# Optimization experiments

Hardware: AMD Instinct MI355X
Metric: run time of the kernel (lower is better)

Reference implementation:

```python
import jax, jax.numpy as jnp
import numpy as np

B, S, E, H = 8, 2048, 1024, 64

def setup_inputs() -> dict:
    key = jax.random.key(0)
    ks = jax.random.split(key, 7)
    scale = 1.0 / np.sqrt(E)
    return {
        "x": jax.random.normal(ks[0], (B, S, E), dtype=jnp.float32),
        "mask": jnp.ones((B, S), dtype=jnp.int32),
        "Wq": jax.random.uniform(ks[1], (E, H), jnp.float32, -scale, scale),
        "bq": jax.random.uniform(ks[2], (H,), jnp.float32, -scale, scale),
        "Wk": jax.random.uniform(ks[3], (E, H), jnp.float32, -scale, scale),
        "bk": jax.random.uniform(ks[4], (H,), jnp.float32, -scale, scale),
        "Wv": jax.random.uniform(ks[5], (E, H), jnp.float32, -scale, scale),
        "bv": jax.random.uniform(ks[6], (H,), jnp.float32, -scale, scale),
    }

def reference(x, mask, Wq, bq, Wk, bk, Wv, bv):
    # q,k,v: [B,S,H]
    q = jnp.einsum('bse,eh->bsh', x, Wq) + bq
    k = jnp.einsum('bse,eh->bsh', x, Wk) + bk
    v = jnp.einsum('bse,eh->bsh', x, Wv) + bv
    # scores: [B,S,S]
    scores = jnp.einsum('bqh,bkh->bqk', q, k) / jnp.sqrt(jnp.asarray(H, q.dtype))
    causal = jnp.tril(jnp.ones((S, S), dtype=bool))  # [S,S]
    pad = (mask != 0)[:, None, :]                    # [B,1,S]
    neg_inf = jnp.asarray(float('-inf'), scores.dtype)
    scores = jnp.where(causal[None] & pad, scores, neg_inf)
    attn = jax.nn.softmax(scores, axis=-1)
    return jnp.einsum('bqk,bkh->bqh', attn, v)
```

## Files before the change

kernel.cpp:

```cpp
#include <hip/hip_runtime.h>
#include <hip/hip_bf16.h>

#define S_ 2048
#define E_ 1024
#define QNC 16

typedef __attribute__((ext_vector_type(8))) short short8;
typedef __attribute__((ext_vector_type(4))) float f32x4;

__device__ __forceinline__ short f2bf(float f) {
    __hip_bfloat16 h = __float2bfloat16(f);
    return *(short*)&h;
}

__device__ __forceinline__ void g2l16(const void* g, void* l) {
    __builtin_amdgcn_global_load_lds(
        (const __attribute__((address_space(1))) void*)g,
        (__attribute__((address_space(3))) void*)l, 16, 0, 0);
}

__global__ __launch_bounds__(256) void prep_weights(
    const float* __restrict__ Wq, const float* __restrict__ Wk,
    const float* __restrict__ Wv, unsigned short* __restrict__ Wt)
{
    int idx = blockIdx.x * 256 + threadIdx.x;
    int n = idx >> 10, k = idx & (E_ - 1);
    const float* W = (n < 64) ? Wq : (n < 128) ? Wk : Wv;
    Wt[idx] = (unsigned short)f2bf(W[k * 64 + (n & 63)]);
}

__global__ __launch_bounds__(256, 2) void qkv_main(
    const float* __restrict__ x, const unsigned short* __restrict__ Wt,
    const float* __restrict__ bq, const float* __restrict__ bk,
    const float* __restrict__ bv,
    unsigned short* __restrict__ Q, unsigned short* __restrict__ K,
    unsigned short* __restrict__ Vt)
{
    __shared__ __align__(16) char pool[2][32768];
    int tid = threadIdx.x;
    int wave = tid >> 6, lane = tid & 63;
    int lo = lane & 15, hi = lane >> 4;
    int wm = wave >> 1, wn = wave & 1;
    int rowbase = blockIdx.x * 32;
    const char* xg = (const char*)x;
    const char* wg = (const char*)Wt;

    f32x4 acc[6];
    #pragma unroll
    for (int j = 0; j < 6; ++j) acc[j] = (f32x4){0.f, 0.f, 0.f, 0.f};

    #define STAGE(bb, kc)                                                         \
        {                                                                         \
            _Pragma("unroll")                                                     \
            for (int i = 0; i < 2; ++i) {                                         \
                int u_lin = i * 256 + tid;                                        \
                int r = u_lin >> 4, u = u_lin & 15;                               \
                const char* src = xg + (size_t)(rowbase + r) * 4096 + (kc) * 256  \
                                  + (((u & 8) | ((u & 7) ^ (r & 7))) << 4);       \
                g2l16(src, &pool[bb][(i * 256 + wave * 64) * 16]);                \
            }                                                                     \
            _Pragma("unroll")                                                     \
            for (int i = 0; i < 6; ++i) {                                         \
                int u_lin = i * 256 + tid;                                        \
                int c = u_lin >> 3, u = u_lin & 7;                                \
                const char* src = wg + (size_t)c * 2048 + (kc) * 128              \
                                  + ((u ^ (c & 7)) << 4);                         \
                g2l16(src, &pool[bb][8192 + (i * 256 + wave * 64) * 16]);         \
            }                                                                     \
        }

    STAGE(0, 0);
    asm volatile("s_waitcnt vmcnt(0)" ::: "memory");
    __builtin_amdgcn_sched_barrier(0);
    __builtin_amdgcn_s_barrier();

    for (int t = 0; t < QNC; ++t) {
        if (t + 1 < QNC) STAGE((t + 1) & 1, t + 1);

        const char* lx = pool[t & 1];
        const char* lw = pool[t & 1] + 8192;
        int r = wm * 16 + lo;
        #pragma unroll
        for (int kk = 0; kk < 2; ++kk) {
            int u0 = kk * 8 + hi * 2;
            float4 a0 = *(const float4*)(lx + r * 256
                + (((u0 & 8) | ((u0 & 7) ^ (r & 7))) << 4));
            float4 a1 = *(const float4*)(lx + r * 256
                + ((((u0 + 1) & 8) | (((u0 + 1) & 7) ^ (r & 7))) << 4));
            short8 af;
            af[0] = f2bf(a0.x); af[1] = f2bf(a0.y);
            af[2] = f2bf(a0.z); af[3] = f2bf(a0.w);
            af[4] = f2bf(a1.x); af[5] = f2bf(a1.y);
            af[6] = f2bf(a1.z); af[7] = f2bf(a1.w);
            #pragma unroll
            for (int j = 0; j < 6; ++j) {
                int c = wn * 96 + j * 16 + lo;
                short8 bf = *(const short8*)(lw + c * 128
                    + (((kk * 4 + hi) ^ (c & 7)) << 4));
                acc[j] = __builtin_amdgcn_mfma_f32_16x16x32_bf16(af, bf, acc[j], 0, 0, 0);
            }
        }

        __builtin_amdgcn_sched_barrier(0);
        asm volatile("s_waitcnt vmcnt(0)" ::: "memory");
        __builtin_amdgcn_sched_barrier(0);
        __builtin_amdgcn_s_barrier();
    }
    #undef STAGE

    char* eq = pool[0];
    unsigned short* ev = (unsigned short*)pool[1];
    #pragma unroll
    for (int j = 0; j < 6; ++j) {
        int n = wn * 96 + j * 16 + lo;
        #pragma unroll
        for (int rr4 = 0; rr4 < 4; ++rr4) {
            int rr = wm * 16 + 4 * hi + rr4;
            float v = acc[j][rr4];
            if (n < 64) {
                *(unsigned short*)(eq + rr * 272 + n * 2) =
                    (unsigned short)f2bf(v + bq[n]);
            } else if (n < 128) {
                *(unsigned short*)(eq + rr * 272 + n * 2) =
                    (unsigned short)f2bf(v + bk[n - 64]);
            } else {
                ev[(n - 128) * 40 + rr] = (unsigned short)f2bf(v + bv[n - 128]);
            }
        }
    }
    __syncthreads();

    {
        #pragma unroll
        for (int i = 0; i < 2; ++i) {
            int u_lin = i * 256 + tid;
            int row = u_lin >> 4, seg = u_lin & 15;
            short8 val = *(const short8*)(eq + row * 272 + seg * 16);
            if (seg < 8)
                *(short8*)(Q + (size_t)(rowbase + row) * 64 + seg * 8) = val;
            else
                *(short8*)(K + (size_t)(rowbase + row) * 64 + (seg - 8) * 8) = val;
        }
        int h = tid >> 2, su = tid & 3;
        int b = rowbase >> 11, sl0 = rowbase & (S_ - 1);
        short8 val = *(const short8*)(ev + h * 40 + su * 8);
        *(short8*)(Vt + ((size_t)(b * 64 + h)) * S_ + sl0 + su * 8) = val;
    }
}

__global__ __launch_bounds__(256) void attn_stage(
    const unsigned short* __restrict__ Q, const unsigned short* __restrict__ K,
    const unsigned short* __restrict__ Vt, const int* __restrict__ mask,
    float* __restrict__ part)
{
    __shared__ __align__(16) char kv[3][16384];
    __shared__ __align__(16) unsigned short p_lds[4][16][72];
    int tid = threadIdx.x;
    int wave = tid >> 6, lane = tid & 63;
    int lo = lane & 15, hi = lane >> 4;
    int blk = blockIdx.x;
    int c = blk & 3;
    int pr = blk >> 2;
    int b = pr & 7;
    int qt64 = 31 - (pr >> 3);
    int nkt = qt64 + 1;
    int chunk = (nkt + 3) >> 2;
    int kt0 = c * chunk;
    int kt1 = min(kt0 + chunk, nkt);
    int ntile = kt1 - kt0;
    int qrow0 = qt64 * 64 + wave * 16;

    f32x4 o[4];
    float ps[4] = {0.f, 0.f, 0.f, 0.f};
    #pragma unroll
    for (int i = 0; i < 4; ++i) o[i] = (f32x4){0.f, 0.f, 0.f, 0.f};

    #define ASTAGE(bb, kt)                                                        \
        {                                                                         \
            int kbase_ = (kt) * 64;                                               \
            const char* kg = (const char*)K + (size_t)(b * S_ + kbase_) * 128;    \
            const char* vg = (const char*)Vt + (size_t)b * 64 * 4096 + kbase_ * 2;\
            _Pragma("unroll")                                                     \
            for (int j = 0; j < 2; ++j) {                                         \
                int r = (j * 4 + wave) * 8 + (lane >> 3);                         \
                int un = lane & 7;                                                \
                g2l16(kg + r * 128 + ((un ^ (r & 7)) << 4),                       \
                      &kv[bb][(j * 4 + wave) * 1024]);                            \
                g2l16(vg + (size_t)r * 4096 + ((un ^ (r & 7)) << 4),              \
                      &kv[bb][8192 + (j * 4 + wave) * 1024]);                     \
            }                                                                     \
        }

    if (ntile > 0) {
        const unsigned short* qp = Q + ((size_t)(b * S_ + qrow0 + lo)) * 64 + 8 * hi;
        short8 qf0 = *(const short8*)(qp);
        short8 qf1 = *(const short8*)(qp + 32);

        unsigned mbits = 0;
        for (int tt = 0; tt < 8; ++tt) {
            if (tt < ntile) {
                int kbase = (kt0 + tt) * 64;
                #pragma unroll
                for (int nt = 0; nt < 4; ++nt)
                    if (mask[b * S_ + kbase + nt * 16 + lo] != 0)
                        mbits |= (1u << (tt * 4 + nt));
            }
        }
        asm volatile("s_waitcnt vmcnt(0)" ::: "memory");
        __builtin_amdgcn_sched_barrier(0);

        ASTAGE(0, kt0);
        if (ntile > 1) ASTAGE(1, kt0 + 1);
        __builtin_amdgcn_sched_barrier(0);
        if (ntile > 1) asm volatile("s_waitcnt vmcnt(4)" ::: "memory");
        else           asm volatile("s_waitcnt vmcnt(0)" ::: "memory");
        __builtin_amdgcn_sched_barrier(0);
        __builtin_amdgcn_s_barrier();

        for (int t = 0; t < ntile; ++t) {
            int kbase = (kt0 + t) * 64;
            const char* kb = kv[t % 3];
            const char* vb = kv[t % 3] + 8192;

            f32x4 s[4];
            #pragma unroll
            for (int i = 0; i < 4; ++i) s[i] = (f32x4){0.f, 0.f, 0.f, 0.f};
            #pragma unroll
            for (int nt = 0; nt < 4; ++nt) {
                short8 kf0 = *(const short8*)(kb + (nt * 16 + lo) * 128 + ((hi ^ (lo & 7)) << 4));
                short8 kf1 = *(const short8*)(kb + (nt * 16 + lo) * 128 + (((4 + hi) ^ (lo & 7)) << 4));
                s[nt] = __builtin_amdgcn_mfma_f32_16x16x32_bf16(qf0, kf0, s[nt], 0, 0, 0);
                s[nt] = __builtin_amdgcn_mfma_f32_16x16x32_bf16(qf1, kf1, s[nt], 0, 0, 0);
            }

            #pragma unroll
            for (int nt = 0; nt < 4; ++nt) {
                int kpos = kbase + nt * 16 + lo;
                bool mok = (mbits >> (t * 4 + nt)) & 1;
                #pragma unroll
                for (int r = 0; r < 4; ++r) {
                    int qpos = qrow0 + 4 * hi + r;
                    bool ok = mok && (kpos <= qpos);
                    float pv = ok ? __expf(s[nt][r] * 0.125f) : 0.f;
                    ps[r] += pv;
                    p_lds[wave][4 * hi + r][nt * 16 + lo] = (unsigned short)f2bf(pv);
                }
            }

            #pragma unroll
            for (int kk = 0; kk < 2; ++kk) {
                short8 pf = *(const short8*)&p_lds[wave][lo][kk * 32 + 8 * hi];
                #pragma unroll
                for (int nt = 0; nt < 4; ++nt) {
                    short8 vf = *(const short8*)(vb + (nt * 16 + lo) * 128
                                                 + (((kk * 4 + hi) ^ (lo & 7)) << 4));
                    o[nt] = __builtin_amdgcn_mfma_f32_16x16x32_bf16(pf, vf, o[nt], 0, 0, 0);
                }
            }

            if (t + 2 < ntile) ASTAGE((t + 2) % 3, kt0 + t + 2);
            __builtin_amdgcn_sched_barrier(0);
            if (t + 1 < ntile) {
                if (t + 2 < ntile) asm volatile("s_waitcnt vmcnt(4)" ::: "memory");
                else               asm volatile("s_waitcnt vmcnt(0)" ::: "memory");
                __builtin_amdgcn_sched_barrier(0);
                __builtin_amdgcn_s_barrier();
            }
        }
    }
    #undef ASTAGE

    float l[4];
    #pragma unroll
    for (int r = 0; r < 4; ++r) {
        float v = ps[r];
        v += __shfl_xor(v, 1);
        v += __shfl_xor(v, 2);
        v += __shfl_xor(v, 4);
        v += __shfl_xor(v, 8);
        l[r] = v;
    }

    int tile16 = b * 128 + qt64 * 4 + wave;
    float* pp = part + (((size_t)c * 1024 + tile16) * 64 + lane) * 20;
    #pragma unroll
    for (int nt = 0; nt < 4; ++nt) *(f32x4*)(pp + nt * 4) = o[nt];
    f32x4 ll;
    #pragma unroll
    for (int r = 0; r < 4; ++r) ll[r] = l[r];
    *(f32x4*)(pp + 16) = ll;
}

__global__ __launch_bounds__(256) void attn_comb(
    const float* __restrict__ part, float* __restrict__ out)
{
    int g = blockIdx.x * 256 + threadIdx.x;
    int tile = g >> 6, lane = g & 63;
    int lo = lane & 15, hi = lane >> 4;
    int b = tile >> 7, qt = tile & 127;
    int qrow0 = qt * 16;

    f32x4 o[4];
    float l[4] = {0.f, 0.f, 0.f, 0.f};
    #pragma unroll
    for (int i = 0; i < 4; ++i) o[i] = (f32x4){0.f, 0.f, 0.f, 0.f};

    #pragma unroll
    for (int c = 0; c < 4; ++c) {
        const float* pp = part + (((size_t)c * 1024 + tile) * 64 + lane) * 20;
        #pragma unroll
        for (int nt = 0; nt < 4; ++nt) {
            f32x4 po = *(const f32x4*)(pp + nt * 4);
            #pragma unroll
            for (int r = 0; r < 4; ++r) o[nt][r] += po[r];
        }
        f32x4 pl = *(const f32x4*)(pp + 16);
        #pragma unroll
        for (int r = 0; r < 4; ++r) l[r] += pl[r];
    }

    #pragma unroll
    for (int nt = 0; nt < 4; ++nt) {
        #pragma unroll
        for (int r = 0; r < 4; ++r) {
            int qpos = qrow0 + 4 * hi + r;
            out[((size_t)(b * S_ + qpos)) * 64 + nt * 16 + lo] =
                (l[r] > 0.f) ? o[nt][r] / l[r] : 0.f;
        }
    }
}

extern "C" void kernel_launch(void* const* d_in, const int* in_sizes, int n_in,
                              void* d_out, int out_size, void* d_ws, size_t ws_size,
                              hipStream_t stream) {
    const float* x   = (const float*)d_in[0];
    const int*   msk = (const int*)d_in[1];
    const float* Wq  = (const float*)d_in[2];
    const float* bq  = (const float*)d_in[3];
    const float* Wk  = (const float*)d_in[4];
    const float* bk  = (const float*)d_in[5];
    const float* Wv  = (const float*)d_in[6];
    const float* bv  = (const float*)d_in[7];
    float* outp = (float*)d_out;

    char* w = (char*)d_ws;
    unsigned short* Wt = (unsigned short*)w;
    unsigned short* Qb = (unsigned short*)(w + 0x080000);
    unsigned short* Kb = (unsigned short*)(w + 0x280000);
    unsigned short* Vt = (unsigned short*)(w + 0x480000);
    float* partp = (float*)(w + 0x680000);

    prep_weights<<<dim3(768), dim3(256), 0, stream>>>(Wq, Wk, Wv, Wt);
    qkv_main<<<dim3(512), dim3(256), 0, stream>>>(x, Wt, bq, bk, bv, Qb, Kb, Vt);
    attn_stage<<<dim3(1024), dim3(256), 0, stream>>>(Qb, Kb, Vt, msk, partp);
    attn_comb<<<dim3(256), dim3(256), 0, stream>>>(partp, outp);
}
```

Before: 58.32 us.

## Split QKV projection columns across two blocks and triple-buffer K-loop staging

The QKV projection kernel now launches twice as many blocks, each computing 96 of the 192 output columns for a 32-row tile, which halves per-block accumulators and weight staging. The LDS pipeline moves from double to triple buffering with a two-stage prefetch and partial vmcnt waits, so loads for chunk t+2 overlap compute on chunk t. The aim is more parallelism and better latency hiding in the memory-bound projection. In exchange, each x tile is now loaded twice (once per column half), which adds global traffic for the dominant input, and the epilogue writes are split by half.

```diff
diff --git a/kernel.cpp b/kernel.cpp
--- a/kernel.cpp
+++ b/kernel.cpp
@@ -36,18 +36,20 @@
     unsigned short* __restrict__ Q, unsigned short* __restrict__ K,
     unsigned short* __restrict__ Vt)
 {
-    __shared__ __align__(16) char pool[2][32768];
+    __shared__ __align__(16) char pool[3][20480];
     int tid = threadIdx.x;
     int wave = tid >> 6, lane = tid & 63;
     int lo = lane & 15, hi = lane >> 4;
     int wm = wave >> 1, wn = wave & 1;
-    int rowbase = blockIdx.x * 32;
+    int rb = blockIdx.x >> 1, ch = blockIdx.x & 1;
+    int rowbase = rb * 32;
+    int colbase = ch * 96;
     const char* xg = (const char*)x;
     const char* wg = (const char*)Wt;
 
-    f32x4 acc[6];
-    #pragma unroll
-    for (int j = 0; j < 6; ++j) acc[j] = (f32x4){0.f, 0.f, 0.f, 0.f};
+    f32x4 acc[3];
+    #pragma unroll
+    for (int j = 0; j < 3; ++j) acc[j] = (f32x4){0.f, 0.f, 0.f, 0.f};
 
     #define STAGE(bb, kc)                                                         \
         {                                                                         \
@@ -60,25 +62,25 @@
                 g2l16(src, &pool[bb][(i * 256 + wave * 64) * 16]);                \
             }                                                                     \
             _Pragma("unroll")                                                     \
-            for (int i = 0; i < 6; ++i) {                                         \
+            for (int i = 0; i < 3; ++i) {                                         \
                 int u_lin = i * 256 + tid;                                        \
-                int c = u_lin >> 3, u = u_lin & 7;                                \
-                const char* src = wg + (size_t)c * 2048 + (kc) * 128              \
-                                  + ((u ^ (c & 7)) << 4);                         \
+                int cl = u_lin >> 3, u = u_lin & 7;                               \
+                const char* src = wg + (size_t)(colbase + cl) * 2048 + (kc) * 128 \
+                                  + ((u ^ (cl & 7)) << 4);                        \
                 g2l16(src, &pool[bb][8192 + (i * 256 + wave * 64) * 16]);         \
             }                                                                     \
         }
 
-    STAGE(0, 0);
-    asm volatile("s_waitcnt vmcnt(0)" ::: "memory");
+    STAGE(0, 0); STAGE(1, 1);
+    asm volatile("s_waitcnt vmcnt(5)" ::: "memory");
     __builtin_amdgcn_sched_barrier(0);
     __builtin_amdgcn_s_barrier();
 
     for (int t = 0; t < QNC; ++t) {
-        if (t + 1 < QNC) STAGE((t + 1) & 1, t + 1);
-
-        const char* lx = pool[t & 1];
-        const char* lw = pool[t & 1] + 8192;
+        if (t + 2 < QNC) STAGE((t + 2) % 3, t + 2);
+
+        const char* lx = pool[t % 3];
+        const char* lw = pool[t % 3] + 8192;
         int r = wm * 16 + lo;
         #pragma unroll
         for (int kk = 0; kk < 2; ++kk) {
@@ -93,35 +95,40 @@
             af[4] = f2bf(a1.x); af[5] = f2bf(a1.y);
             af[6] = f2bf(a1.z); af[7] = f2bf(a1.w);
             #pragma unroll
-            for (int j = 0; j < 6; ++j) {
-                int c = wn * 96 + j * 16 + lo;
-                short8 bf = *(const short8*)(lw + c * 128
-                    + (((kk * 4 + hi) ^ (c & 7)) << 4));
+            for (int j = 0; j < 3; ++j) {
+                int cl = wn * 48 + j * 16 + lo;
+                short8 bf = *(const short8*)(lw + cl * 128
+                    + (((kk * 4 + hi) ^ (cl & 7)) << 4));
                 acc[j] = __builtin_amdgcn_mfma_f32_16x16x32_bf16(af, bf, acc[j], 0, 0, 0);
             }
         }
 
         __builtin_amdgcn_sched_barrier(0);
-        asm volatile("s_waitcnt vmcnt(0)" ::: "memory");
-        __builtin_amdgcn_sched_barrier(0);
-        __builtin_amdgcn_s_barrier();
+        if (t + 2 < QNC)      asm volatile("s_waitcnt vmcnt(5)" ::: "memory");
+        else if (t + 1 < QNC) asm volatile("s_waitcnt vmcnt(0)" ::: "memory");
+        if (t + 1 < QNC) {
+            __builtin_amdgcn_sched_barrier(0);
+            __builtin_amdgcn_s_barrier();
+        }
     }
     #undef STAGE
 
+    __syncthreads();
     char* eq = pool[0];
     unsigned short* ev = (unsigned short*)pool[1];
     #pragma unroll
-    for (int j = 0; j < 6; ++j) {
-        int n = wn * 96 + j * 16 + lo;
-        #pragma unroll
-        for (int rr4 = 0; rr4 < 4; ++rr4) {
-            int rr = wm * 16 + 4 * hi + rr4;
-            float v = acc[j][rr4];
+    for (int j = 0; j < 3; ++j) {
+        int nl = wn * 48 + j * 16 + lo;
+        int n = colbase + nl;
+        #pragma unroll
+        for (int r4 = 0; r4 < 4; ++r4) {
+            int rr = wm * 16 + 4 * hi + r4;
+            float v = acc[j][r4];
             if (n < 64) {
-                *(unsigned short*)(eq + rr * 272 + n * 2) =
+                *(unsigned short*)(eq + rr * 208 + nl * 2) =
                     (unsigned short)f2bf(v + bq[n]);
             } else if (n < 128) {
-                *(unsigned short*)(eq + rr * 272 + n * 2) =
+                *(unsigned short*)(eq + rr * 208 + nl * 2) =
                     (unsigned short)f2bf(v + bk[n - 64]);
             } else {
                 ev[(n - 128) * 40 + rr] = (unsigned short)f2bf(v + bv[n - 128]);
@@ -130,21 +137,29 @@
     }
     __syncthreads();
 
-    {
-        #pragma unroll
-        for (int i = 0; i < 2; ++i) {
-            int u_lin = i * 256 + tid;
-            int row = u_lin >> 4, seg = u_lin & 15;
-            short8 val = *(const short8*)(eq + row * 272 + seg * 16);
-            if (seg < 8)
-                *(short8*)(Q + (size_t)(rowbase + row) * 64 + seg * 8) = val;
-            else
-                *(short8*)(K + (size_t)(rowbase + row) * 64 + (seg - 8) * 8) = val;
-        }
-        int h = tid >> 2, su = tid & 3;
-        int b = rowbase >> 11, sl0 = rowbase & (S_ - 1);
-        short8 val = *(const short8*)(ev + h * 40 + su * 8);
-        *(short8*)(Vt + ((size_t)(b * 64 + h)) * S_ + sl0 + su * 8) = val;
+    if (ch == 0) {
+        {
+            int row = tid >> 3, seg = tid & 7;
+            short8 val = *(const short8*)(eq + row * 208 + seg * 16);
+            *(short8*)(Q + (size_t)(rowbase + row) * 64 + seg * 8) = val;
+        }
+        if (tid < 128) {
+            int row = tid >> 2, seg = tid & 3;
+            short8 val = *(const short8*)(eq + row * 208 + 128 + seg * 16);
+            *(short8*)(K + (size_t)(rowbase + row) * 64 + seg * 8) = val;
+        }
+    } else {
+        if (tid < 128) {
+            int row = tid >> 2, seg = tid & 3;
+            short8 val = *(const short8*)(eq + row * 208 + seg * 16);
+            *(short8*)(K + (size_t)(rowbase + row) * 64 + 32 + seg * 8) = val;
+        }
+        {
+            int h = tid >> 2, su = tid & 3;
+            int b = rowbase >> 11, sl0 = rowbase & (S_ - 1);
+            short8 val = *(const short8*)(ev + h * 40 + su * 8);
+            *(short8*)(Vt + ((size_t)(b * 64 + h)) * S_ + sl0 + su * 8) = val;
+        }
     }
 }
 
@@ -351,7 +366,7 @@
     float* partp = (float*)(w + 0x680000);
 
     prep_weights<<<dim3(768), dim3(256), 0, stream>>>(Wq, Wk, Wv, Wt);
-    qkv_main<<<dim3(512), dim3(256), 0, stream>>>(x, Wt, bq, bk, bv, Qb, Kb, Vt);
+    qkv_main<<<dim3(1024), dim3(256), 0, stream>>>(x, Wt, bq, bk, bv, Qb, Kb, Vt);
     attn_stage<<<dim3(1024), dim3(256), 0, stream>>>(Qb, Kb, Vt, msk, partp);
     attn_comb<<<dim3(256), dim3(256), 0, stream>>>(partp, outp);
 }
```

Result: slower. 76.03 us (+30.4%).

## Double QKV projection row tile and use triple-buffered prefetch

Applied to the files above, without the earlier changes.

The QKV projection kernel now processes 64 rows per block instead of 32. Each wave computes two 16-row tiles that reuse the same loaded weight fragments, which halves weight LDS and global traffic per row. The LDS pipeline moves from double to triple buffering with two stages in flight, using partial vmcnt waits. In exchange the grid shrinks to 256 blocks at one block per CU, lowering occupancy and parallelism on a 256-CU part.

```diff
diff --git a/kernel.cpp b/kernel.cpp
--- a/kernel.cpp
+++ b/kernel.cpp
@@ -29,30 +29,32 @@
     Wt[idx] = (unsigned short)f2bf(W[k * 64 + (n & 63)]);
 }
 
-__global__ __launch_bounds__(256, 2) void qkv_main(
+__global__ __launch_bounds__(256, 1) void qkv_main(
     const float* __restrict__ x, const unsigned short* __restrict__ Wt,
     const float* __restrict__ bq, const float* __restrict__ bk,
     const float* __restrict__ bv,
     unsigned short* __restrict__ Q, unsigned short* __restrict__ K,
     unsigned short* __restrict__ Vt)
 {
-    __shared__ __align__(16) char pool[2][32768];
+    __shared__ __align__(16) char pool[3][40960];
     int tid = threadIdx.x;
     int wave = tid >> 6, lane = tid & 63;
     int lo = lane & 15, hi = lane >> 4;
     int wm = wave >> 1, wn = wave & 1;
-    int rowbase = blockIdx.x * 32;
+    int rowbase = blockIdx.x * 64;
     const char* xg = (const char*)x;
     const char* wg = (const char*)Wt;
 
-    f32x4 acc[6];
-    #pragma unroll
-    for (int j = 0; j < 6; ++j) acc[j] = (f32x4){0.f, 0.f, 0.f, 0.f};
+    f32x4 acc[2][6];
+    #pragma unroll
+    for (int a = 0; a < 2; ++a)
+        #pragma unroll
+        for (int j = 0; j < 6; ++j) acc[a][j] = (f32x4){0.f, 0.f, 0.f, 0.f};
 
     #define STAGE(bb, kc)                                                         \
         {                                                                         \
             _Pragma("unroll")                                                     \
-            for (int i = 0; i < 2; ++i) {                                         \
+            for (int i = 0; i < 4; ++i) {                                         \
                 int u_lin = i * 256 + tid;                                        \
                 int r = u_lin >> 4, u = u_lin & 15;                               \
                 const char* src = xg + (size_t)(rowbase + r) * 4096 + (kc) * 256  \
@@ -62,69 +64,83 @@
             _Pragma("unroll")                                                     \
             for (int i = 0; i < 6; ++i) {                                         \
                 int u_lin = i * 256 + tid;                                        \
-                int c = u_lin >> 3, u = u_lin & 7;                                \
-                const char* src = wg + (size_t)c * 2048 + (kc) * 128              \
-                                  + ((u ^ (c & 7)) << 4);                         \
-                g2l16(src, &pool[bb][8192 + (i * 256 + wave * 64) * 16]);         \
+                int cl = u_lin >> 3, u = u_lin & 7;                               \
+                const char* src = wg + (size_t)cl * 2048 + (kc) * 128             \
+                                  + ((u ^ (cl & 7)) << 4);                        \
+                g2l16(src, &pool[bb][16384 + (i * 256 + wave * 64) * 16]);        \
             }                                                                     \
         }
 
-    STAGE(0, 0);
-    asm volatile("s_waitcnt vmcnt(0)" ::: "memory");
+    STAGE(0, 0); STAGE(1, 1);
+    asm volatile("s_waitcnt vmcnt(10)" ::: "memory");
     __builtin_amdgcn_sched_barrier(0);
     __builtin_amdgcn_s_barrier();
 
     for (int t = 0; t < QNC; ++t) {
-        if (t + 1 < QNC) STAGE((t + 1) & 1, t + 1);
-
-        const char* lx = pool[t & 1];
-        const char* lw = pool[t & 1] + 8192;
-        int r = wm * 16 + lo;
+        if (t + 2 < QNC) STAGE((t + 2) % 3, t + 2);
+
+        const char* lx = pool[t % 3];
+        const char* lw = pool[t % 3] + 16384;
         #pragma unroll
         for (int kk = 0; kk < 2; ++kk) {
-            int u0 = kk * 8 + hi * 2;
-            float4 a0 = *(const float4*)(lx + r * 256
-                + (((u0 & 8) | ((u0 & 7) ^ (r & 7))) << 4));
-            float4 a1 = *(const float4*)(lx + r * 256
-                + ((((u0 + 1) & 8) | (((u0 + 1) & 7) ^ (r & 7))) << 4));
-            short8 af;
-            af[0] = f2bf(a0.x); af[1] = f2bf(a0.y);
-            af[2] = f2bf(a0.z); af[3] = f2bf(a0.w);
-            af[4] = f2bf(a1.x); af[5] = f2bf(a1.y);
-            af[6] = f2bf(a1.z); af[7] = f2bf(a1.w);
+            short8 bf[6];
             #pragma unroll
             for (int j = 0; j < 6; ++j) {
-                int c = wn * 96 + j * 16 + lo;
-                short8 bf = *(const short8*)(lw + c * 128
-                    + (((kk * 4 + hi) ^ (c & 7)) << 4));
-                acc[j] = __builtin_amdgcn_mfma_f32_16x16x32_bf16(af, bf, acc[j], 0, 0, 0);
+                int cl = wn * 96 + j * 16 + lo;
+                bf[j] = *(const short8*)(lw + cl * 128
+                    + (((kk * 4 + hi) ^ (cl & 7)) << 4));
+            }
+            #pragma unroll
+            for (int rt = 0; rt < 2; ++rt) {
+                int r = wm * 32 + rt * 16 + lo;
+                int u0 = kk * 8 + hi * 2;
+                float4 a0 = *(const float4*)(lx + r * 256
+                    + (((u0 & 8) | ((u0 & 7) ^ (r & 7))) << 4));
+                float4 a1 = *(const float4*)(lx + r * 256
+                    + ((((u0 + 1) & 8) | (((u0 + 1) & 7) ^ (r & 7))) << 4));
+                short8 af;
+                af[0] = f2bf(a0.x); af[1] = f2bf(a0.y);
+                af[2] = f2bf(a0.z); af[3] = f2bf(a0.w);
+                af[4] = f2bf(a1.x); af[5] = f2bf(a1.y);
+                af[6] = f2bf(a1.z); af[7] = f2bf(a1.w);
+                #pragma unroll
+                for (int j = 0; j < 6; ++j)
+                    acc[rt][j] = __builtin_amdgcn_mfma_f32_16x16x32_bf16(
+                        af, bf[j], acc[rt][j], 0, 0, 0);
             }
         }
 
         __builtin_amdgcn_sched_barrier(0);
-        asm volatile("s_waitcnt vmcnt(0)" ::: "memory");
-        __builtin_amdgcn_sched_barrier(0);
-        __builtin_amdgcn_s_barrier();
+        if (t + 2 < QNC)      asm volatile("s_waitcnt vmcnt(10)" ::: "memory");
+        else if (t + 1 < QNC) asm volatile("s_waitcnt vmcnt(0)" ::: "memory");
+        if (t + 1 < QNC) {
+            __builtin_amdgcn_sched_barrier(0);
+            __builtin_amdgcn_s_barrier();
+        }
     }
     #undef STAGE
 
+    __syncthreads();
     char* eq = pool[0];
-    unsigned short* ev = (unsigned short*)pool[1];
-    #pragma unroll
-    for (int j = 0; j < 6; ++j) {
-        int n = wn * 96 + j * 16 + lo;
-        #pragma unroll
-        for (int rr4 = 0; rr4 < 4; ++rr4) {
-            int rr = wm * 16 + 4 * hi + rr4;
-            float v = acc[j][rr4];
-            if (n < 64) {
-                *(unsigned short*)(eq + rr * 272 + n * 2) =
-                    (unsigned short)f2bf(v + bq[n]);
-            } else if (n < 128) {
-                *(unsigned short*)(eq + rr * 272 + n * 2) =
-                    (unsigned short)f2bf(v + bk[n - 64]);
-            } else {
-                ev[(n - 128) * 40 + rr] = (unsigned short)f2bf(v + bv[n - 128]);
+    unsigned short* ev = (unsigned short*)pool[2];
+    #pragma unroll
+    for (int rt = 0; rt < 2; ++rt) {
+        #pragma unroll
+        for (int j = 0; j < 6; ++j) {
+            int n = wn * 96 + j * 16 + lo;
+            #pragma unroll
+            for (int r4 = 0; r4 < 4; ++r4) {
+                int rr = wm * 32 + rt * 16 + 4 * hi + r4;
+                float v = acc[rt][j][r4];
+                if (n < 64) {
+                    *(unsigned short*)(eq + rr * 272 + n * 2) =
+                        (unsigned short)f2bf(v + bq[n]);
+                } else if (n < 128) {
+                    *(unsigned short*)(eq + rr * 272 + n * 2) =
+                        (unsigned short)f2bf(v + bk[n - 64]);
+                } else {
+                    ev[(n - 128) * 72 + rr] = (unsigned short)f2bf(v + bv[n - 128]);
+                }
             }
         }
     }
@@ -132,7 +148,7 @@
 
     {
         #pragma unroll
-        for (int i = 0; i < 2; ++i) {
+        for (int i = 0; i < 4; ++i) {
             int u_lin = i * 256 + tid;
             int row = u_lin >> 4, seg = u_lin & 15;
             short8 val = *(const short8*)(eq + row * 272 + seg * 16);
@@ -141,10 +157,14 @@
             else
                 *(short8*)(K + (size_t)(rowbase + row) * 64 + (seg - 8) * 8) = val;
         }
-        int h = tid >> 2, su = tid & 3;
         int b = rowbase >> 11, sl0 = rowbase & (S_ - 1);
-        short8 val = *(const short8*)(ev + h * 40 + su * 8);
-        *(short8*)(Vt + ((size_t)(b * 64 + h)) * S_ + sl0 + su * 8) = val;
+        #pragma unroll
+        for (int i = 0; i < 2; ++i) {
+            int u_lin = i * 256 + tid;
+            int h = u_lin >> 3, su = u_lin & 7;
+            short8 val = *(const short8*)(ev + h * 72 + su * 8);
+            *(short8*)(Vt + ((size_t)(b * 64 + h)) * S_ + sl0 + su * 8) = val;
+        }
     }
 }
 
@@ -351,7 +371,7 @@
     float* partp = (float*)(w + 0x680000);
 
     prep_weights<<<dim3(768), dim3(256), 0, stream>>>(Wq, Wk, Wv, Wt);
-    qkv_main<<<dim3(512), dim3(256), 0, stream>>>(x, Wt, bq, bk, bv, Qb, Kb, Vt);
+    qkv_main<<<dim3(256), dim3(256), 0, stream>>>(x, Wt, bq, bk, bv, Qb, Kb, Vt);
     attn_stage<<<dim3(1024), dim3(256), 0, stream>>>(Qb, Kb, Vt, msk, partp);
     attn_comb<<<dim3(256), dim3(256), 0, stream>>>(partp, outp);
 }
```

After: 65.83 us. 12.9% more time.

## Halve QKV projection row tile and K-chunk to raise occupancy

Applied to the files above, without the earlier changes.

The QKV projection kernel now processes 16 rows per block instead of 32 and stages 32-element K chunks, giving 32 pipeline steps instead of 16. Each of the four waves owns 48 output columns. LDS per block shrinks to about 28KB, which lets the launch bounds ask for 4 blocks per CU, and the grid doubles to 1024 blocks. The aim is more parallelism and better latency hiding. In exchange, every block reloads the full bf16 weight matrix, so total weight traffic through L2 doubles, and there are more barrier steps per row. The V-transpose LDS buffer now uses an 18-element row stride, so its 16-byte reads are not 16-byte aligned.

```diff
diff --git a/kernel.cpp b/kernel.cpp
--- a/kernel.cpp
+++ b/kernel.cpp
@@ -3,7 +3,7 @@
 
 #define S_ 2048
 #define E_ 1024
-#define QNC 16
+#define QNC 32
 
 typedef __attribute__((ext_vector_type(8))) short short8;
 typedef __attribute__((ext_vector_type(4))) float f32x4;
@@ -29,43 +29,41 @@
     Wt[idx] = (unsigned short)f2bf(W[k * 64 + (n & 63)]);
 }
 
-__global__ __launch_bounds__(256, 2) void qkv_main(
+__global__ __launch_bounds__(256, 4) void qkv_main(
     const float* __restrict__ x, const unsigned short* __restrict__ Wt,
     const float* __restrict__ bq, const float* __restrict__ bk,
     const float* __restrict__ bv,
     unsigned short* __restrict__ Q, unsigned short* __restrict__ K,
     unsigned short* __restrict__ Vt)
 {
-    __shared__ __align__(16) char pool[2][32768];
+    __shared__ __align__(16) char pool[2][14336];
     int tid = threadIdx.x;
     int wave = tid >> 6, lane = tid & 63;
     int lo = lane & 15, hi = lane >> 4;
-    int wm = wave >> 1, wn = wave & 1;
-    int rowbase = blockIdx.x * 32;
+    int wn = wave;
+    int rowbase = blockIdx.x * 16;
     const char* xg = (const char*)x;
     const char* wg = (const char*)Wt;
 
-    f32x4 acc[6];
-    #pragma unroll
-    for (int j = 0; j < 6; ++j) acc[j] = (f32x4){0.f, 0.f, 0.f, 0.f};
+    f32x4 acc[3];
+    #pragma unroll
+    for (int j = 0; j < 3; ++j) acc[j] = (f32x4){0.f, 0.f, 0.f, 0.f};
 
     #define STAGE(bb, kc)                                                         \
         {                                                                         \
-            _Pragma("unroll")                                                     \
-            for (int i = 0; i < 2; ++i) {                                         \
-                int u_lin = i * 256 + tid;                                        \
-                int r = u_lin >> 4, u = u_lin & 15;                               \
-                const char* src = xg + (size_t)(rowbase + r) * 4096 + (kc) * 256  \
-                                  + (((u & 8) | ((u & 7) ^ (r & 7))) << 4);       \
-                g2l16(src, &pool[bb][(i * 256 + wave * 64) * 16]);                \
+            if (tid < 128) {                                                      \
+                int r = tid >> 3, u = tid & 7;                                    \
+                const char* src = xg + (size_t)(rowbase + r) * 4096 + (kc) * 128  \
+                                  + ((u ^ (r & 7)) << 4);                         \
+                g2l16(src, &pool[bb][wave * 1024]);                               \
             }                                                                     \
             _Pragma("unroll")                                                     \
-            for (int i = 0; i < 6; ++i) {                                         \
-                int u_lin = i * 256 + tid;                                        \
-                int c = u_lin >> 3, u = u_lin & 7;                                \
-                const char* src = wg + (size_t)c * 2048 + (kc) * 128              \
-                                  + ((u ^ (c & 7)) << 4);                         \
-                g2l16(src, &pool[bb][8192 + (i * 256 + wave * 64) * 16]);         \
+            for (int i = 0; i < 3; ++i) {                                         \
+                int w_ = i * 256 + tid;                                           \
+                int cl = w_ >> 2, u = w_ & 3;                                     \
+                const char* src = wg + (size_t)cl * 2048 + (kc) * 64              \
+                                  + ((u ^ ((cl ^ (cl >> 2)) & 3)) << 4);          \
+                g2l16(src, &pool[bb][2048 + (i * 256 + wave * 64) * 16]);         \
             }                                                                     \
         }
 
@@ -78,27 +76,28 @@
         if (t + 1 < QNC) STAGE((t + 1) & 1, t + 1);
 
         const char* lx = pool[t & 1];
-        const char* lw = pool[t & 1] + 8192;
-        int r = wm * 16 + lo;
-        #pragma unroll
-        for (int kk = 0; kk < 2; ++kk) {
-            int u0 = kk * 8 + hi * 2;
-            float4 a0 = *(const float4*)(lx + r * 256
-                + (((u0 & 8) | ((u0 & 7) ^ (r & 7))) << 4));
-            float4 a1 = *(const float4*)(lx + r * 256
-                + ((((u0 + 1) & 8) | (((u0 + 1) & 7) ^ (r & 7))) << 4));
+        const char* lw = pool[t & 1] + 2048;
+
+        short8 bf[3];
+        #pragma unroll
+        for (int j = 0; j < 3; ++j) {
+            int cl = wn * 48 + j * 16 + lo;
+            bf[j] = *(const short8*)(lw + cl * 64
+                + ((hi ^ ((cl ^ (cl >> 2)) & 3)) << 4));
+        }
+        {
+            int r = lo;
+            int u0 = 2 * hi;
+            float4 a0 = *(const float4*)(lx + r * 128 + ((u0 ^ (r & 7)) << 4));
+            float4 a1 = *(const float4*)(lx + r * 128 + (((u0 + 1) ^ (r & 7)) << 4));
             short8 af;
             af[0] = f2bf(a0.x); af[1] = f2bf(a0.y);
             af[2] = f2bf(a0.z); af[3] = f2bf(a0.w);
             af[4] = f2bf(a1.x); af[5] = f2bf(a1.y);
             af[6] = f2bf(a1.z); af[7] = f2bf(a1.w);
             #pragma unroll
-            for (int j = 0; j < 6; ++j) {
-                int c = wn * 96 + j * 16 + lo;
-                short8 bf = *(const short8*)(lw + c * 128
-                    + (((kk * 4 + hi) ^ (c & 7)) << 4));
-                acc[j] = __builtin_amdgcn_mfma_f32_16x16x32_bf16(af, bf, acc[j], 0, 0, 0);
-            }
+            for (int j = 0; j < 3; ++j)
+                acc[j] = __builtin_amdgcn_mfma_f32_16x16x32_bf16(af, bf[j], acc[j], 0, 0, 0);
         }
 
         __builtin_amdgcn_sched_barrier(0);
@@ -108,15 +107,16 @@
     }
     #undef STAGE
 
+    __syncthreads();
     char* eq = pool[0];
     unsigned short* ev = (unsigned short*)pool[1];
     #pragma unroll
-    for (int j = 0; j < 6; ++j) {
-        int n = wn * 96 + j * 16 + lo;
-        #pragma unroll
-        for (int rr4 = 0; rr4 < 4; ++rr4) {
-            int rr = wm * 16 + 4 * hi + rr4;
-            float v = acc[j][rr4];
+    for (int j = 0; j < 3; ++j) {
+        int n = wn * 48 + j * 16 + lo;
+        #pragma unroll
+        for (int r4 = 0; r4 < 4; ++r4) {
+            int rr = 4 * hi + r4;
+            float v = acc[j][r4];
             if (n < 64) {
                 *(unsigned short*)(eq + rr * 272 + n * 2) =
                     (unsigned short)f2bf(v + bq[n]);
@@ -124,26 +124,24 @@
                 *(unsigned short*)(eq + rr * 272 + n * 2) =
                     (unsigned short)f2bf(v + bk[n - 64]);
             } else {
-                ev[(n - 128) * 40 + rr] = (unsigned short)f2bf(v + bv[n - 128]);
+                ev[(n - 128) * 18 + rr] = (unsigned short)f2bf(v + bv[n - 128]);
             }
         }
     }
     __syncthreads();
 
     {
-        #pragma unroll
-        for (int i = 0; i < 2; ++i) {
-            int u_lin = i * 256 + tid;
-            int row = u_lin >> 4, seg = u_lin & 15;
-            short8 val = *(const short8*)(eq + row * 272 + seg * 16);
-            if (seg < 8)
-                *(short8*)(Q + (size_t)(rowbase + row) * 64 + seg * 8) = val;
-            else
-                *(short8*)(K + (size_t)(rowbase + row) * 64 + (seg - 8) * 8) = val;
-        }
-        int h = tid >> 2, su = tid & 3;
+        int row = tid >> 4, seg = tid & 15;
+        short8 val = *(const short8*)(eq + row * 272 + seg * 16);
+        if (seg < 8)
+            *(short8*)(Q + (size_t)(rowbase + row) * 64 + seg * 8) = val;
+        else
+            *(short8*)(K + (size_t)(rowbase + row) * 64 + (seg - 8) * 8) = val;
+    }
+    if (tid < 128) {
+        int h = tid >> 1, su = tid & 1;
         int b = rowbase >> 11, sl0 = rowbase & (S_ - 1);
-        short8 val = *(const short8*)(ev + h * 40 + su * 8);
+        short8 val = *(const short8*)((const char*)ev + h * 36 + su * 16);
         *(short8*)(Vt + ((size_t)(b * 64 + h)) * S_ + sl0 + su * 8) = val;
     }
 }
@@ -351,7 +349,7 @@
     float* partp = (float*)(w + 0x680000);
 
     prep_weights<<<dim3(768), dim3(256), 0, stream>>>(Wq, Wk, Wv, Wt);
-    qkv_main<<<dim3(512), dim3(256), 0, stream>>>(x, Wt, bq, bk, bv, Qb, Kb, Vt);
+    qkv_main<<<dim3(1024), dim3(256), 0, stream>>>(x, Wt, bq, bk, bv, Qb, Kb, Vt);
     attn_stage<<<dim3(1024), dim3(256), 0, stream>>>(Qb, Kb, Vt, msk, partp);
     attn_comb<<<dim3(256), dim3(256), 0, stream>>>(partp, outp);
 }
```

After: 66.50 us. +14.0%, slower.
